# Performance work log

Measured on AMD Instinct MI355X. Metric: run time of the kernel, lower is better.

Reference implementation:

```python
import jax, jax.numpy as jnp
import numpy as np

OUT = 56          # roi_align / mask resolution
SCALE = 0.25      # spatial_scale (bases at stride 4)
CO = 14           # raw coefficient resolution


def _roi_align_one(feat, box):
    """torchvision roi_align, aligned=True, sampling_ratio=1.
    feat: [B, H, W] base maps for this roi's image; box: [4] = (x0,y0,x1,y1).
    Returns [B, OUT, OUT]."""
    H, W = feat.shape[1], feat.shape[2]
    s = box * SCALE - 0.5  # aligned=True half-pixel offset
    x0, y0, x1, y1 = s[0], s[1], s[2], s[3]
    bw = (x1 - x0) / OUT
    bh = (y1 - y0) / OUT
    # sampling_ratio=1 -> single sample at each bin center
    xs = x0 + (jnp.arange(OUT, dtype=feat.dtype) + 0.5) * bw
    ys = y0 + (jnp.arange(OUT, dtype=feat.dtype) + 0.5) * bh
    vy = (ys >= -1.0) & (ys <= H)
    vx = (xs >= -1.0) & (xs <= W)
    yc = jnp.clip(ys, 0.0, H - 1)
    xc = jnp.clip(xs, 0.0, W - 1)
    yl = jnp.clip(jnp.floor(yc).astype(jnp.int32), 0, H - 2); yh = yl + 1
    xl = jnp.clip(jnp.floor(xc).astype(jnp.int32), 0, W - 2); xh = xl + 1
    ly = yc - yl; hy = 1.0 - ly
    lx = xc - xl; hx = 1.0 - lx
    fll = feat[:, yl, :][:, :, xl]; flh = feat[:, yl, :][:, :, xh]
    fhl = feat[:, yh, :][:, :, xl]; fhh = feat[:, yh, :][:, :, xh]
    val = (hy[:, None] * (hx[None, :] * fll + lx[None, :] * flh)
           + ly[:, None] * (hx[None, :] * fhl + lx[None, :] * fhh))
    return val * (vy[:, None] & vx[None, :])


def _paste_masks(masks, boxes, img_h, img_w):
    """do_paste_mask: grid_sample(bilinear, align_corners=False, zero pad).
    The grid is separable (y depends on row, x on column), so express it as two
    batched matmuls with tent-kernel weights. masks: [N,56,56] -> [N,img_h,img_w]."""
    x0, y0, x1, y1 = (boxes[:, 0:1], boxes[:, 1:2], boxes[:, 2:3], boxes[:, 3:4])
    gy = ((jnp.arange(img_h, dtype=masks.dtype) + 0.5 - y0) / (y1 - y0)) * 2.0 - 1.0  # [N,H]
    gx = ((jnp.arange(img_w, dtype=masks.dtype) + 0.5 - x0) / (x1 - x0)) * 2.0 - 1.0  # [N,W]
    # unnormalize (align_corners=False): f = (g+1)*size/2 - 0.5
    fy = (gy + 1.0) * OUT * 0.5 - 0.5
    fx = (gx + 1.0) * OUT * 0.5 - 0.5
    idx = jnp.arange(OUT, dtype=masks.dtype)
    Wy = jnp.maximum(0.0, 1.0 - jnp.abs(fy[:, :, None] - idx))  # [N, img_h, 56]
    Wx = jnp.maximum(0.0, 1.0 - jnp.abs(fx[:, :, None] - idx))  # [N, img_w, 56]
    rows = jnp.einsum('nhm,nmw->nhw', Wy, masks)                # [N, img_h, 56]
    return jnp.einsum('nhw,nqw->nhq', rows, Wx)                 # [N, img_h, img_w]


def setup_inputs() -> dict:
    key = jax.random.key(0)
    ks = jax.random.split(key, 6)
    b_h, b_w = 136, 200                 # bases at stride 4 of a 544x800 image
    img_h, img_w = b_h * 4, b_w * 4
    N, Bb = 100, 4
    bases = jax.random.normal(ks[0], (1, Bb, b_h, b_w), jnp.float32)
    x0 = jax.random.uniform(ks[1], (N, 1), minval=0.0, maxval=img_w * 0.55)
    y0 = jax.random.uniform(ks[2], (N, 1), minval=0.0, maxval=img_h * 0.55)
    w = jax.random.uniform(ks[3], (N, 1), minval=32.0, maxval=img_w * 0.4)
    h = jax.random.uniform(ks[4], (N, 1), minval=32.0, maxval=img_h * 0.4)
    boxes = jnp.concatenate([x0, y0,
                             jnp.minimum(x0 + w, img_w - 1.0),
                             jnp.minimum(y0 + h, img_h - 1.0)], axis=1)
    top = jax.random.normal(ks[5], (N, Bb * CO * CO), jnp.float32)
    box_feat = jnp.concatenate([jnp.zeros((N, 1), jnp.float32), boxes, top], axis=1)
    return {"bases": bases, "box_feat": box_feat}


def reference(bases, box_feat):
    bidx = box_feat[:, 0].astype(jnp.int32)
    boxes = box_feat[:, 1:5]
    top_feat = box_feat[:, 5:]
    N = box_feat.shape[0]
    Bb, b_h, b_w = bases.shape[1], bases.shape[2], bases.shape[3]
    # roi_align over all detections
    rois = jax.vmap(lambda i, b: _roi_align_one(bases[i], b))(bidx, boxes)  # [N,B,56,56]
    # merge_bases: upsample 14->56 (bilinear, align_corners=False), softmax over bases, blend
    coeffs = top_feat.reshape(N, Bb, CO, CO)
    coeffs = jax.image.resize(coeffs, (N, Bb, OUT, OUT), method='bilinear')
    coeffs = jax.nn.softmax(coeffs, axis=1)
    masks = jax.nn.sigmoid(jnp.sum(rois * coeffs, axis=1))  # [N,56,56]
    return _paste_masks(masks, boxes, b_h * 4, b_w * 4)      # [N, 4*b_h, 4*b_w]
```

## Files before the change

kernel.cpp:

```cpp
#include <hip/hip_runtime.h>
#include <math.h>

#define OUTD 56
#define COD  14
#define BH   136
#define BW   200
#define IMGH 544
#define IMGW 800
#define BB   4
#define BFS  789

__global__ __launch_bounds__(256) void mask_kernel(
    const float* __restrict__ bases,
    const float* __restrict__ box_feat,
    float* __restrict__ masks) {
  const int n = blockIdx.x;
  const float* bf = box_feat + (size_t)n * BFS;
  const int bidx = (int)bf[0];
  const float x0 = bf[1], y0 = bf[2], x1 = bf[3], y1 = bf[4];
  const float sx0 = x0 * 0.25f - 0.5f;
  const float sy0 = y0 * 0.25f - 0.5f;
  const float bw = (x1 - x0) * 0.25f * (1.0f / OUTD);
  const float bh = (y1 - y0) * 0.25f * (1.0f / OUTD);
  const float* feat = bases + (size_t)bidx * BB * BH * BW;
  const float* top  = bf + 5;

  for (int p = threadIdx.x; p < OUTD * OUTD; p += blockDim.x) {
    const int y = p / OUTD;
    const int x = p - y * OUTD;

    const float ysv = sy0 + ((float)y + 0.5f) * bh;
    const float xsv = sx0 + ((float)x + 0.5f) * bw;
    const float valid =
        (ysv >= -1.0f && ysv <= (float)BH && xsv >= -1.0f && xsv <= (float)BW)
            ? 1.0f : 0.0f;
    const float yc = fminf(fmaxf(ysv, 0.0f), (float)(BH - 1));
    const float xc = fminf(fmaxf(xsv, 0.0f), (float)(BW - 1));
    int yl = (int)floorf(yc); yl = yl > (BH - 2) ? (BH - 2) : yl;
    int xl = (int)floorf(xc); xl = xl > (BW - 2) ? (BW - 2) : xl;
    const float ly = yc - (float)yl, hy = 1.0f - ly;
    const float lx = xc - (float)xl, hx = 1.0f - lx;
    const float w00 = hy * hx, w01 = hy * lx, w10 = ly * hx, w11 = ly * lx;

    float cyf = fminf(fmaxf(((float)y + 0.5f) * 0.25f - 0.5f, 0.0f), (float)(COD - 1));
    float cxf = fminf(fmaxf(((float)x + 0.5f) * 0.25f - 0.5f, 0.0f), (float)(COD - 1));
    int cyl = (int)floorf(cyf); cyl = cyl > (COD - 2) ? (COD - 2) : cyl;
    int cxl = (int)floorf(cxf); cxl = cxl > (COD - 2) ? (COD - 2) : cxl;
    const float cly = cyf - (float)cyl, chy = 1.0f - cly;
    const float clx = cxf - (float)cxl, chx = 1.0f - clx;
    const float cw00 = chy * chx, cw01 = chy * clx, cw10 = cly * chx, cw11 = cly * clx;

    float rvals[BB], cvals[BB];
#pragma unroll
    for (int b = 0; b < BB; ++b) {
      const float* fb = feat + b * BH * BW;
      const float r = w00 * fb[yl * BW + xl]       + w01 * fb[yl * BW + xl + 1] +
                      w10 * fb[(yl + 1) * BW + xl] + w11 * fb[(yl + 1) * BW + xl + 1];
      rvals[b] = r * valid;
      const float* tb = top + b * COD * COD;
      cvals[b] = cw00 * tb[cyl * COD + cxl]       + cw01 * tb[cyl * COD + cxl + 1] +
                 cw10 * tb[(cyl + 1) * COD + cxl] + cw11 * tb[(cyl + 1) * COD + cxl + 1];
    }

    const float mx = fmaxf(fmaxf(cvals[0], cvals[1]), fmaxf(cvals[2], cvals[3]));
    float e[BB], s = 0.0f;
#pragma unroll
    for (int b = 0; b < BB; ++b) { e[b] = __expf(cvals[b] - mx); s += e[b]; }
    const float inv = 1.0f / s;
    float dot = 0.0f;
#pragma unroll
    for (int b = 0; b < BB; ++b) dot += rvals[b] * (e[b] * inv);
    const float mval = 1.0f / (1.0f + __expf(-dot));

    masks[(size_t)n * (OUTD * OUTD) + p] = mval;
  }
}

__global__ __launch_bounds__(256) void paste_kernel(
    const float* __restrict__ masks,
    const float* __restrict__ box_feat,
    float4* __restrict__ out, int total4) {
  const int t = blockIdx.x * blockDim.x + threadIdx.x;
  if (t >= total4) return;
  const int per_n = IMGH * (IMGW / 4);
  const int n   = t / per_n;
  const int rem = t - n * per_n;
  const int h   = rem / (IMGW / 4);
  const int q4  = rem - h * (IMGW / 4);

  const float* bf = box_feat + (size_t)n * BFS;
  const float x0 = bf[1], y0 = bf[2], x1 = bf[3], y1 = bf[4];

  const float fy = ((float)h + 0.5f - y0) * ((float)OUTD / (y1 - y0)) - 0.5f;

  float4 o = make_float4(0.0f, 0.0f, 0.0f, 0.0f);
  if (fy > -1.0f && fy < (float)OUTD) {
    const int ml = (int)floorf(fy);
    const float wy1 = fy - (float)ml;
    const float wy0 = 1.0f - wy1;
    const float* mk = masks + (size_t)n * (OUTD * OUTD);
    const bool r0v = (ml >= 0);
    const bool r1v = (ml + 1 <= OUTD - 1);
    const float* row0 = mk + (r0v ? ml : 0) * OUTD;
    const float* row1 = mk + (r1v ? (ml + 1) : 0) * OUTD;
    const float invw = (float)OUTD / (x1 - x0);

    float res[4];
#pragma unroll
    for (int i = 0; i < 4; ++i) {
      const int q = q4 * 4 + i;
      const float fx = ((float)q + 0.5f - x0) * invw - 0.5f;
      float v = 0.0f;
      if (fx > -1.0f && fx < (float)OUTD) {
        const int xl = (int)floorf(fx);
        const float wx1 = fx - (float)xl;
        const float wx0 = 1.0f - wx1;
        const bool xlv = (xl >= 0);
        const bool xhv = (xl + 1 <= OUTD - 1);
        const int xls = xlv ? xl : 0;
        const int xhs = xhv ? (xl + 1) : 0;
        float v00 = (r0v && xlv) ? row0[xls] : 0.0f;
        float v01 = (r0v && xhv) ? row0[xhs] : 0.0f;
        float v10 = (r1v && xlv) ? row1[xls] : 0.0f;
        float v11 = (r1v && xhv) ? row1[xhs] : 0.0f;
        v = wy0 * (wx0 * v00 + wx1 * v01) + wy1 * (wx0 * v10 + wx1 * v11);
      }
      res[i] = v;
    }
    o = make_float4(res[0], res[1], res[2], res[3]);
  }
  out[t] = o;
}

extern "C" void kernel_launch(void* const* d_in, const int* in_sizes, int n_in,
                              void* d_out, int out_size, void* d_ws, size_t ws_size,
                              hipStream_t stream) {
  const float* bases    = (const float*)d_in[0];
  const float* box_feat = (const float*)d_in[1];
  const int N = in_sizes[1] / BFS;

  float* masks = (float*)d_ws;

  mask_kernel<<<N, 256, 0, stream>>>(bases, box_feat, masks);

  const int total4 = N * IMGH * (IMGW / 4);
  const int blocks = (total4 + 255) / 256;
  paste_kernel<<<blocks, 256, 0, stream>>>(masks, box_feat, (float4*)d_out, total4);
}
```

Baseline: 182.4 us.

## Fuse mask blending into paste kernel with per-row shared mask recompute

Measured after the change: 198.2 us. 8.6% more time.

```diff
diff --git a/kernel.cpp b/kernel.cpp
--- a/kernel.cpp
+++ b/kernel.cpp
@@ -10,126 +10,125 @@
 #define BB   4
 #define BFS  789
 
-__global__ __launch_bounds__(256) void mask_kernel(
+
+__device__ __forceinline__ float mask_value(
+    const float* __restrict__ feat,
+    const float* __restrict__ top,
+    float sx0, float sy0, float bw, float bh,
+    int y, int x) {
+  const float ysv = sy0 + ((float)y + 0.5f) * bh;
+  const float xsv = sx0 + ((float)x + 0.5f) * bw;
+  const float valid =
+      (ysv >= -1.0f && ysv <= (float)BH && xsv >= -1.0f && xsv <= (float)BW)
+          ? 1.0f : 0.0f;
+  const float yc = fminf(fmaxf(ysv, 0.0f), (float)(BH - 1));
+  const float xc = fminf(fmaxf(xsv, 0.0f), (float)(BW - 1));
+  int yl = (int)floorf(yc); yl = yl > (BH - 2) ? (BH - 2) : yl;
+  int xl = (int)floorf(xc); xl = xl > (BW - 2) ? (BW - 2) : xl;
+  const float ly = yc - (float)yl, hy = 1.0f - ly;
+  const float lx = xc - (float)xl, hx = 1.0f - lx;
+  const float w00 = hy * hx, w01 = hy * lx, w10 = ly * hx, w11 = ly * lx;
+
+  float cyf = fminf(fmaxf(((float)y + 0.5f) * 0.25f - 0.5f, 0.0f), (float)(COD - 1));
+  float cxf = fminf(fmaxf(((float)x + 0.5f) * 0.25f - 0.5f, 0.0f), (float)(COD - 1));
+  int cyl = (int)floorf(cyf); cyl = cyl > (COD - 2) ? (COD - 2) : cyl;
+  int cxl = (int)floorf(cxf); cxl = cxl > (COD - 2) ? (COD - 2) : cxl;
+  const float cly = cyf - (float)cyl, chy = 1.0f - cly;
+  const float clx = cxf - (float)cxl, chx = 1.0f - clx;
+  const float cw00 = chy * chx, cw01 = chy * clx, cw10 = cly * chx, cw11 = cly * clx;
+
+  float rvals[BB], cvals[BB];
+#pragma unroll
+  for (int b = 0; b < BB; ++b) {
+    const float* fb = feat + b * BH * BW;
+    const float r = w00 * fb[yl * BW + xl]       + w01 * fb[yl * BW + xl + 1] +
+                    w10 * fb[(yl + 1) * BW + xl] + w11 * fb[(yl + 1) * BW + xl + 1];
+    rvals[b] = r * valid;
+    const float* tb = top + b * COD * COD;
+    cvals[b] = cw00 * tb[cyl * COD + cxl]       + cw01 * tb[cyl * COD + cxl + 1] +
+               cw10 * tb[(cyl + 1) * COD + cxl] + cw11 * tb[(cyl + 1) * COD + cxl + 1];
+  }
+
+  const float mx = fmaxf(fmaxf(cvals[0], cvals[1]), fmaxf(cvals[2], cvals[3]));
+  float e[BB], s = 0.0f;
+#pragma unroll
+  for (int b = 0; b < BB; ++b) { e[b] = __expf(cvals[b] - mx); s += e[b]; }
+  const float inv = 1.0f / s;
+  float dot = 0.0f;
+#pragma unroll
+  for (int b = 0; b < BB; ++b) dot += rvals[b] * (e[b] * inv);
+  return 1.0f / (1.0f + __expf(-dot));
+}
+
+__global__ __launch_bounds__(256) void fused_blend_paste(
     const float* __restrict__ bases,
     const float* __restrict__ box_feat,
-    float* __restrict__ masks) {
-  const int n = blockIdx.x;
-  const float* bf = box_feat + (size_t)n * BFS;
-  const int bidx = (int)bf[0];
-  const float x0 = bf[1], y0 = bf[2], x1 = bf[3], y1 = bf[4];
-  const float sx0 = x0 * 0.25f - 0.5f;
-  const float sy0 = y0 * 0.25f - 0.5f;
-  const float bw = (x1 - x0) * 0.25f * (1.0f / OUTD);
-  const float bh = (y1 - y0) * 0.25f * (1.0f / OUTD);
-  const float* feat = bases + (size_t)bidx * BB * BH * BW;
-  const float* top  = bf + 5;
-
-  for (int p = threadIdx.x; p < OUTD * OUTD; p += blockDim.x) {
-    const int y = p / OUTD;
-    const int x = p - y * OUTD;
-
-    const float ysv = sy0 + ((float)y + 0.5f) * bh;
-    const float xsv = sx0 + ((float)x + 0.5f) * bw;
-    const float valid =
-        (ysv >= -1.0f && ysv <= (float)BH && xsv >= -1.0f && xsv <= (float)BW)
-            ? 1.0f : 0.0f;
-    const float yc = fminf(fmaxf(ysv, 0.0f), (float)(BH - 1));
-    const float xc = fminf(fmaxf(xsv, 0.0f), (float)(BW - 1));
-    int yl = (int)floorf(yc); yl = yl > (BH - 2) ? (BH - 2) : yl;
-    int xl = (int)floorf(xc); xl = xl > (BW - 2) ? (BW - 2) : xl;
-    const float ly = yc - (float)yl, hy = 1.0f - ly;
-    const float lx = xc - (float)xl, hx = 1.0f - lx;
-    const float w00 = hy * hx, w01 = hy * lx, w10 = ly * hx, w11 = ly * lx;
-
-    float cyf = fminf(fmaxf(((float)y + 0.5f) * 0.25f - 0.5f, 0.0f), (float)(COD - 1));
-    float cxf = fminf(fmaxf(((float)x + 0.5f) * 0.25f - 0.5f, 0.0f), (float)(COD - 1));
-    int cyl = (int)floorf(cyf); cyl = cyl > (COD - 2) ? (COD - 2) : cyl;
-    int cxl = (int)floorf(cxf); cxl = cxl > (COD - 2) ? (COD - 2) : cxl;
-    const float cly = cyf - (float)cyl, chy = 1.0f - cly;
-    const float clx = cxf - (float)cxl, chx = 1.0f - clx;
-    const float cw00 = chy * chx, cw01 = chy * clx, cw10 = cly * chx, cw11 = cly * clx;
-
-    float rvals[BB], cvals[BB];
-#pragma unroll
-    for (int b = 0; b < BB; ++b) {
-      const float* fb = feat + b * BH * BW;
-      const float r = w00 * fb[yl * BW + xl]       + w01 * fb[yl * BW + xl + 1] +
-                      w10 * fb[(yl + 1) * BW + xl] + w11 * fb[(yl + 1) * BW + xl + 1];
-      rvals[b] = r * valid;
-      const float* tb = top + b * COD * COD;
-      cvals[b] = cw00 * tb[cyl * COD + cxl]       + cw01 * tb[cyl * COD + cxl + 1] +
-                 cw10 * tb[(cyl + 1) * COD + cxl] + cw11 * tb[(cyl + 1) * COD + cxl + 1];
-    }
-
-    const float mx = fmaxf(fmaxf(cvals[0], cvals[1]), fmaxf(cvals[2], cvals[3]));
-    float e[BB], s = 0.0f;
-#pragma unroll
-    for (int b = 0; b < BB; ++b) { e[b] = __expf(cvals[b] - mx); s += e[b]; }
-    const float inv = 1.0f / s;
-    float dot = 0.0f;
-#pragma unroll
-    for (int b = 0; b < BB; ++b) dot += rvals[b] * (e[b] * inv);
-    const float mval = 1.0f / (1.0f + __expf(-dot));
-
-    masks[(size_t)n * (OUTD * OUTD) + p] = mval;
-  }
-}
-
-__global__ __launch_bounds__(256) void paste_kernel(
-    const float* __restrict__ masks,
-    const float* __restrict__ box_feat,
-    float4* __restrict__ out, int total4) {
-  const int t = blockIdx.x * blockDim.x + threadIdx.x;
-  if (t >= total4) return;
-  const int per_n = IMGH * (IMGW / 4);
-  const int n   = t / per_n;
-  const int rem = t - n * per_n;
-  const int h   = rem / (IMGW / 4);
-  const int q4  = rem - h * (IMGW / 4);
+    float4* __restrict__ out) {
+  const int h = blockIdx.x;
+  const int n = blockIdx.y;
+  const int tid = threadIdx.x;
 
   const float* bf = box_feat + (size_t)n * BFS;
   const float x0 = bf[1], y0 = bf[2], x1 = bf[3], y1 = bf[4];
 
+  float4* orow = out + ((size_t)n * IMGH + h) * (IMGW / 4);
   const float fy = ((float)h + 0.5f - y0) * ((float)OUTD / (y1 - y0)) - 0.5f;
 
-  float4 o = make_float4(0.0f, 0.0f, 0.0f, 0.0f);
-  if (fy > -1.0f && fy < (float)OUTD) {
-    const int ml = (int)floorf(fy);
-    const float wy1 = fy - (float)ml;
-    const float wy0 = 1.0f - wy1;
-    const float* mk = masks + (size_t)n * (OUTD * OUTD);
-    const bool r0v = (ml >= 0);
-    const bool r1v = (ml + 1 <= OUTD - 1);
-    const float* row0 = mk + (r0v ? ml : 0) * OUTD;
-    const float* row1 = mk + (r1v ? (ml + 1) : 0) * OUTD;
-    const float invw = (float)OUTD / (x1 - x0);
+  if (!(fy > -1.0f && fy < (float)OUTD)) {
+    if (tid < IMGW / 4) orow[tid] = make_float4(0.f, 0.f, 0.f, 0.f);
+    return;
+  }
 
-    float res[4];
+  const int ml = (int)floorf(fy);
+  const float wy1 = fy - (float)ml;
+  const float wy0 = 1.0f - wy1;
+
+  __shared__ float mrow[2][OUTD];
+
+  if (tid < 2 * OUTD) {
+    const int r_idx = (tid >= OUTD) ? 1 : 0;
+    const int x = tid - r_idx * OUTD;
+    const int r = ml + r_idx;
+    float val = 0.0f;
+    if (r >= 0 && r < OUTD) {
+      const int bidx = (int)bf[0];
+      const float sx0 = x0 * 0.25f - 0.5f;
+      const float sy0 = y0 * 0.25f - 0.5f;
+      const float bwv = (x1 - x0) * 0.25f * (1.0f / OUTD);
+      const float bhv = (y1 - y0) * 0.25f * (1.0f / OUTD);
+      const float* feat = bases + (size_t)bidx * BB * BH * BW;
+      val = mask_value(feat, bf + 5, sx0, sy0, bwv, bhv, r, x);
+    }
+    mrow[r_idx][x] = val;
+  }
+  __syncthreads();
+
+  if (tid >= IMGW / 4) return;
+
+  const float invw = (float)OUTD / (x1 - x0);
+  float res[4];
 #pragma unroll
-    for (int i = 0; i < 4; ++i) {
-      const int q = q4 * 4 + i;
-      const float fx = ((float)q + 0.5f - x0) * invw - 0.5f;
-      float v = 0.0f;
-      if (fx > -1.0f && fx < (float)OUTD) {
-        const int xl = (int)floorf(fx);
-        const float wx1 = fx - (float)xl;
-        const float wx0 = 1.0f - wx1;
-        const bool xlv = (xl >= 0);
-        const bool xhv = (xl + 1 <= OUTD - 1);
-        const int xls = xlv ? xl : 0;
-        const int xhs = xhv ? (xl + 1) : 0;
-        float v00 = (r0v && xlv) ? row0[xls] : 0.0f;
-        float v01 = (r0v && xhv) ? row0[xhs] : 0.0f;
-        float v10 = (r1v && xlv) ? row1[xls] : 0.0f;
-        float v11 = (r1v && xhv) ? row1[xhs] : 0.0f;
-        v = wy0 * (wx0 * v00 + wx1 * v01) + wy1 * (wx0 * v10 + wx1 * v11);
-      }
-      res[i] = v;
+  for (int i = 0; i < 4; ++i) {
+    const int q = tid * 4 + i;
+    const float fx = ((float)q + 0.5f - x0) * invw - 0.5f;
+    float v = 0.0f;
+    if (fx > -1.0f && fx < (float)OUTD) {
+      const int xl = (int)floorf(fx);
+      const float wx1 = fx - (float)xl;
+      const float wx0 = 1.0f - wx1;
+      const bool xlv = (xl >= 0);
+      const bool xhv = (xl + 1 <= OUTD - 1);
+      const int xls = xlv ? xl : 0;
+      const int xhs = xhv ? (xl + 1) : 0;
+      const float v00 = xlv ? mrow[0][xls] : 0.0f;
+      const float v01 = xhv ? mrow[0][xhs] : 0.0f;
+      const float v10 = xlv ? mrow[1][xls] : 0.0f;
+      const float v11 = xhv ? mrow[1][xhs] : 0.0f;
+      v = wy0 * (wx0 * v00 + wx1 * v01) + wy1 * (wx0 * v10 + wx1 * v11);
     }
-    o = make_float4(res[0], res[1], res[2], res[3]);
+    res[i] = v;
   }
-  out[t] = o;
+  orow[tid] = make_float4(res[0], res[1], res[2], res[3]);
 }
 
 extern "C" void kernel_launch(void* const* d_in, const int* in_sizes, int n_in,
@@ -139,11 +138,6 @@
   const float* box_feat = (const float*)d_in[1];
   const int N = in_sizes[1] / BFS;
 
-  float* masks = (float*)d_ws;
-
-  mask_kernel<<<N, 256, 0, stream>>>(bases, box_feat, masks);
-
-  const int total4 = N * IMGH * (IMGW / 4);
-  const int blocks = (total4 + 255) / 256;
-  paste_kernel<<<blocks, 256, 0, stream>>>(masks, box_feat, (float4*)d_out, total4);
+  dim3 grid(IMGH, N);
+  fused_blend_paste<<<grid, 256, 0, stream>>>(bases, box_feat, (float4*)d_out);
 }
```
